# Performance work log

Measured on AMD Instinct MI355X. Metric: run time of the kernel, lower is better.

Reference implementation:

```python
import jax, jax.numpy as jnp
import numpy as np

TOTAL_DIM = 64  # 16+16+16+8+8
HIDDEN = 4 * TOTAL_DIM
NUM_HEADS = 8


def _fourier(x, num_freqs):
    # Dyadic Fourier features: sin/cos of 2^j * x for j in [0, num_freqs).
    # Output dim = input_dim * num_freqs * 2 (matches embed_dim in the module).
    freqs = 2.0 ** jnp.arange(num_freqs, dtype=x.dtype)  # (F,)
    phase = x[..., :, None] * freqs                       # (..., in, F)
    out = jnp.concatenate([jnp.sin(phase), jnp.cos(phase)], axis=-1)  # (..., in, 2F)
    return out.reshape(x.shape[:-1] + (-1,))


def setup_inputs() -> dict:
    key = jax.random.key(0)
    k1, k2, k3, k4, k5, k6 = jax.random.split(key, 6)
    B, Nq, Nk, D = 8, 256, 256, 10
    query_states = jax.random.normal(k1, (B, Nq, D), dtype=jnp.float32)
    key_states = jax.random.normal(k2, (B, Nk, D), dtype=jnp.float32)
    W1 = jax.random.normal(k3, (TOTAL_DIM, HIDDEN), dtype=jnp.float32) / np.sqrt(TOTAL_DIM)
    b1 = jnp.zeros((HIDDEN,), dtype=jnp.float32)
    W2 = jax.random.normal(k4, (HIDDEN, NUM_HEADS), dtype=jnp.float32) / np.sqrt(HIDDEN)
    b2 = jnp.zeros((NUM_HEADS,), dtype=jnp.float32)
    return {"query_states": query_states, "key_states": key_states,
            "W1": W1, "b1": b1, "W2": W2, "b2": b2}


def _features(query_states, key_states):
    # Slice per-ship fields, then broadcast pairwise: q -> (B,Nq,1,*), k -> (B,1,Nk,*)
    q_team = query_states[:, :, None, 0]          # (B,Nq,1)
    k_team = key_states[:, None, :, 0]            # (B,1,Nk)
    q_pos = query_states[:, :, None, 3:5]
    k_pos = key_states[:, None, :, 3:5]
    q_vel = query_states[:, :, None, 5:7]
    k_vel = key_states[:, None, :, 5:7]
    q_att = query_states[:, :, None, 7:9]
    k_att = key_states[:, None, :, 7:9]

    delta_pos = k_pos - q_pos                     # (B,Nq,Nk,2)
    delta_vel = k_vel - q_vel                     # (B,Nq,Nk,2)
    feat_delta_input = jnp.concatenate([delta_pos, delta_vel], axis=-1)  # (B,Nq,Nk,4)

    dist_sq = jnp.sum(delta_pos ** 2, axis=-1, keepdims=True)
    dist = jnp.sqrt(dist_sq + 1e-6)
    inv_dist = 1.0 / (dist + 0.1)
    feat_dist_input = jnp.concatenate([dist, inv_dist], axis=-1)         # (B,Nq,Nk,2)

    bearing = delta_pos / (dist + 1e-6)
    ata = jnp.sum(bearing * q_att, axis=-1, keepdims=True)
    aspect = jnp.sum(bearing * k_att, axis=-1, keepdims=True)
    feat_angle_input = jnp.concatenate([ata, aspect], axis=-1)           # (B,Nq,Nk,2)

    dot_dp_dv = jnp.sum(delta_pos * delta_vel, axis=-1, keepdims=True)
    speed_sq = jnp.sum(delta_vel ** 2, axis=-1, keepdims=True)
    ttca = jnp.tanh(jax.nn.relu(-dot_dp_dv / (speed_sq + 1e-6)))
    feat_intercept_input = jnp.concatenate([ttca, dist], axis=-1)        # (B,Nq,Nk,2)

    same_team = (q_team == k_team).astype(query_states.dtype)[..., None]
    q_speed = jnp.linalg.norm(q_vel, axis=-1, keepdims=True)
    k_speed = jnp.linalg.norm(k_vel, axis=-1, keepdims=True)
    delta_speed = k_speed - q_speed
    feat_team_input = jnp.concatenate([same_team, delta_speed], axis=-1)  # (B,Nq,Nk,2)

    out_dist = _fourier(feat_dist_input, 4)        # 16
    out_angle = _fourier(feat_angle_input, 4)      # 16
    out_delta = _fourier(feat_delta_input, 2)      # 16
    out_intercept = _fourier(feat_intercept_input, 2)  # 8
    out_team = _fourier(feat_team_input, 2)        # 8
    return jnp.concatenate([out_dist, out_angle, out_delta, out_intercept, out_team], axis=-1)


def reference(query_states, key_states, W1, b1, W2, b2):
    combined = _features(query_states, key_states)          # (B,Nq,Nk,64)
    h = jax.nn.silu(combined @ W1 + b1)                     # (B,Nq,Nk,256)
    bias = h @ W2 + b2                                      # (B,Nq,Nk,H)
    return jnp.transpose(bias, (0, 3, 1, 2))                # (B,H,Nq,Nk)
```

## Files before the change

kernel.cpp:

```cpp
#include <hip/hip_runtime.h>
#include <math.h>

#define NB 8
#define NQ 256
#define NK 256
#define DIN 10
#define FDIM 64
#define HIDDEN 256
#define NH 8
#define ROWS_PER_BLK 4

#define FSTRIDE 64
#define HSTRIDE 264

typedef float f32x4 __attribute__((ext_vector_type(4)));
typedef float f32x2 __attribute__((ext_vector_type(2)));
typedef short bf16x8 __attribute__((ext_vector_type(8)));

__device__ __forceinline__ short f2bf(float f) {
    return (short)((__float_as_uint(f) + 0x8000u) >> 16);
}
__device__ __forceinline__ unsigned cvtpk(float a, float b) {
    unsigned r;
    asm("v_cvt_pk_bf16_f32 %0, %1, %2" : "=v"(r) : "v"(a), "v"(b));
    return r;
}
__device__ __forceinline__ float rcpf(float x) { return __builtin_amdgcn_rcpf(x); }
__device__ __forceinline__ float ex2f(float x) { return __builtin_amdgcn_exp2f(x); }
__device__ __forceinline__ float sqtf(float x) { return __builtin_amdgcn_sqrtf(x); }

__device__ __forceinline__ void four4(float x, float* dst) {
    float s1 = __sinf(x), c1 = __cosf(x);
    float s2 = 2.f * s1 * c1, c2 = 1.f - 2.f * s1 * s1;
    float s4 = 2.f * s2 * c2, c4 = 1.f - 2.f * s2 * s2;
    float s8 = 2.f * s4 * c4, c8 = 1.f - 2.f * s4 * s4;
    dst[0] = s1; dst[1] = s2; dst[2] = s4; dst[3] = s8;
    dst[4] = c1; dst[5] = c2; dst[6] = c4; dst[7] = c8;
}
__device__ __forceinline__ void four2(float x, float* dst) {
    float s1 = __sinf(x), c1 = __cosf(x);
    dst[0] = s1; dst[1] = 2.f * s1 * c1;
    dst[2] = c1; dst[3] = 1.f - 2.f * s1 * s1;
}

__global__ __launch_bounds__(512, 4) void relfeat_mfma_kernel(
    const float* __restrict__ q, const float* __restrict__ k,
    const float* __restrict__ W1, const float* __restrict__ b1,
    const float* __restrict__ W2, const float* __restrict__ b2,
    float* __restrict__ out)
{
    __shared__ __align__(16) short feat_s[NK * FSTRIDE];
    __shared__ __align__(16) short h_s[64 * HSTRIDE];

    const int t = threadIdx.x;
    const int wave = t >> 6;
    const int lane15 = t & 15;
    const int quad = (t >> 4) & 3;
    const int p = t & 255;
    const int half = t >> 8;
    const int b = blockIdx.x >> 6;
    const int i0 = (blockIdx.x & 63) * ROWS_PER_BLK;

    const float* kp = k + ((size_t)b * NK + p) * DIN;
    const float k0 = kp[0], k3 = kp[3], k4 = kp[4], k5 = kp[5], k6 = kp[6],
                k7 = kp[7], k8 = kp[8];
    const float k_speed = sqtf(k5 * k5 + k6 * k6);

    bf16x8 w2f[8];
    if (wave < 4) {
#pragma unroll
        for (int ks = 0; ks < 8; ++ks) {
            const float* wp = W2 + (size_t)(ks * 32 + quad * 8) * NH + (lane15 & 7);
            bf16x8 v;
#pragma unroll
            for (int e = 0; e < 8; ++e)
                v[e] = f2bf(-0.69314718f * wp[(size_t)e * NH]);
            w2f[ks] = v;
        }
    }

    const int n0 = wave * 32;
    bf16x8 w1f[2][2];
#pragma unroll
    for (int nt = 0; nt < 2; ++nt)
#pragma unroll
        for (int ks = 0; ks < 2; ++ks) {
            const float* wp = W1 + (size_t)(ks * 32 + quad * 8) * HIDDEN
                              + (n0 + nt * 16 + lane15);
            bf16x8 v;
#pragma unroll
            for (int e = 0; e < 8; ++e)
                v[e] = f2bf(-1.44269504f * wp[(size_t)e * HIDDEN]);
            w1f[nt][ks] = v;
        }
    f32x4 b1c[2];
#pragma unroll
    for (int nt = 0; nt < 2; ++nt) {
        float4 bb = *(const float4*)&b1[n0 + nt * 16 + quad * 4];
        b1c[nt] = (f32x4){-1.44269504f * bb.x, -1.44269504f * bb.y,
                          -1.44269504f * bb.z, -1.44269504f * bb.w};
    }
    const float b2v = (lane15 < NH) ? b2[lane15] : 0.f;
    float* const outp = out + ((size_t)b * NH + (lane15 & 7)) * NQ * NK
                        + wave * 16 + quad * 4;

    const int sw = p & 7;
    const int swr = lane15 & 7;
    const f32x2 one2 = {1.f, 1.f};

#pragma unroll 1
    for (int row = 0; row < ROWS_PER_BLK; ++row) {
        const int i = i0 + row;

        {
            const float* qp = q + ((size_t)b * NQ + i) * DIN;
            const float q0 = qp[0], q3 = qp[3], q4 = qp[4], q5 = qp[5],
                        q6 = qp[6], q7 = qp[7], q8 = qp[8];

            const float dpx = k3 - q3, dpy = k4 - q4;
            const float dvx = k5 - q5, dvy = k6 - q6;
            const float dist = sqtf(dpx * dpx + dpy * dpy + 1e-6f);

            float feat[32];
            if (half == 0) {
                const float inv_dist = rcpf(dist + 0.1f);
                const float dot_dp_dv = dpx * dvx + dpy * dvy;
                const float speed_sq = dvx * dvx + dvy * dvy;
                const float z = fmaxf(0.f, -dot_dp_dv * rcpf(speed_sq + 1e-6f));
                const float ttca = 1.f - 2.f * rcpf(1.f + ex2f(2.88539008f * z));
                const float q_speed = sqtf(q5 * q5 + q6 * q6);
                const float delta_speed = k_speed - q_speed;
                four4(dist,     feat + 0);
                four4(inv_dist, feat + 8);
                four2(ttca,     feat + 16);
                feat[20] = feat[0]; feat[21] = feat[1];
                feat[22] = feat[4]; feat[23] = feat[5];
                const bool st = (q0 == k0);
                feat[24] = st ? 0.84147098f : 0.f;
                feat[25] = st ? 0.90929743f : 0.f;
                feat[26] = st ? 0.54030231f : 1.f;
                feat[27] = st ? -0.41614684f : 1.f;
                four2(delta_speed, feat + 28);
            } else {
                const float inv_d2 = rcpf(dist + 1e-6f);
                const float bear_x = dpx * inv_d2, bear_y = dpy * inv_d2;
                const float ata = bear_x * q7 + bear_y * q8;
                const float aspect = bear_x * k7 + bear_y * k8;
                four4(ata,    feat + 0);
                four4(aspect, feat + 8);
                four2(dpx,    feat + 16);
                four2(dpy,    feat + 20);
                four2(dvx,    feat + 24);
                four2(dvy,    feat + 28);
            }
#pragma unroll
            for (int j = 0; j < 4; ++j) {
                const int c8 = half ? (j + 2) : (j < 2 ? j : j + 4);
                uint4 v;
                v.x = cvtpk(feat[j * 8 + 0], feat[j * 8 + 1]);
                v.y = cvtpk(feat[j * 8 + 2], feat[j * 8 + 3]);
                v.z = cvtpk(feat[j * 8 + 4], feat[j * 8 + 5]);
                v.w = cvtpk(feat[j * 8 + 6], feat[j * 8 + 7]);
                *(uint4*)&feat_s[p * FSTRIDE + ((c8 ^ sw) * 8)] = v;
            }
        }
        __syncthreads();

#pragma unroll 1
        for (int c = 0; c < 4; ++c) {
            const int p0 = c * 64;

            f32x4 acc[2][4];
#pragma unroll
            for (int mt = 0; mt < 4; ++mt) {
                const int r2 = p0 + mt * 16 + lane15;
                const bf16x8 fb = *(const bf16x8*)
                    &feat_s[r2 * FSTRIDE + ((quad ^ swr) * 8)];
                acc[0][mt] = __builtin_amdgcn_mfma_f32_16x16x32_bf16(
                    w1f[0][0], fb, b1c[0], 0, 0, 0);
                acc[1][mt] = __builtin_amdgcn_mfma_f32_16x16x32_bf16(
                    w1f[1][0], fb, b1c[1], 0, 0, 0);
            }
#pragma unroll
            for (int mt = 0; mt < 4; ++mt) {
                const int r2 = p0 + mt * 16 + lane15;
                const bf16x8 fb = *(const bf16x8*)
                    &feat_s[r2 * FSTRIDE + (((4 + quad) ^ swr) * 8)];
#pragma unroll
                for (int nt = 0; nt < 2; ++nt)
                    acc[nt][mt] = __builtin_amdgcn_mfma_f32_16x16x32_bf16(
                        w1f[nt][1], fb, acc[nt][mt], 0, 0, 0);
            }

            uint2 pk[2][4];
#pragma unroll
            for (int nt = 0; nt < 2; ++nt)
#pragma unroll
                for (int mt = 0; mt < 4; ++mt) {
                    const f32x4 a = acc[nt][mt];
                    const f32x2 a01 = {a[0], a[1]}, a23 = {a[2], a[3]};
                    const f32x2 e01 = {ex2f(a[0]), ex2f(a[1])};
                    const f32x2 e23 = {ex2f(a[2]), ex2f(a[3])};
                    const f32x2 t01 = e01 + one2;
                    const f32x2 t23 = e23 + one2;
                    const f32x2 r01 = {rcpf(t01[0]), rcpf(t01[1])};
                    const f32x2 r23 = {rcpf(t23[0]), rcpf(t23[1])};
                    const f32x2 s01 = a01 * r01;
                    const f32x2 s23 = a23 * r23;
                    pk[nt][mt].x = cvtpk(s01[0], s01[1]);
                    pk[nt][mt].y = cvtpk(s23[0], s23[1]);
                }

            __syncthreads();

#pragma unroll
            for (int nt = 0; nt < 2; ++nt)
#pragma unroll
                for (int mt = 0; mt < 4; ++mt) {
                    const int pair = mt * 16 + lane15;
                    const int hbase = n0 + nt * 16 + quad * 4;
                    *(uint2*)&h_s[pair * HSTRIDE + hbase] = pk[nt][mt];
                }
            __syncthreads();

            if (wave < 4) {
                const int pw = wave * 16;
                f32x4 acc2 = (f32x4){b2v, b2v, b2v, b2v};
#pragma unroll
                for (int ks = 0; ks < 8; ++ks) {
                    const bf16x8 ha = *(const bf16x8*)&h_s[(pw + lane15) * HSTRIDE
                                                            + ks * 32 + quad * 8];
                    acc2 = __builtin_amdgcn_mfma_f32_16x16x32_bf16(ha, w2f[ks], acc2, 0, 0, 0);
                }
                if (lane15 < NH) {
                    float* op = outp + (size_t)i * NK + p0;
                    *(float4*)op = make_float4(acc2[0], acc2[1], acc2[2], acc2[3]);
                }
            }
        }
    }
}

extern "C" void kernel_launch(void* const* d_in, const int* in_sizes, int n_in,
                              void* d_out, int out_size, void* d_ws, size_t ws_size,
                              hipStream_t stream) {
    const float* q  = (const float*)d_in[0];
    const float* k  = (const float*)d_in[1];
    const float* W1 = (const float*)d_in[2];
    const float* b1 = (const float*)d_in[3];
    const float* W2 = (const float*)d_in[4];
    const float* b2 = (const float*)d_in[5];
    float* out = (float*)d_out;

    dim3 grid(NB * NQ / ROWS_PER_BLK);
    dim3 block(512);
    relfeat_mfma_kernel<<<grid, block, 0, stream>>>(q, k, W1, b1, W2, b2, out);
}
```

Measured before the change: 107.7 us.

## Double-buffer hidden activations and defer second GEMM to overlap with next chunk

The hidden-activation LDS buffer is split into two, and each chunk's second GEMM (W2 projection plus output store) is deferred into the next chunk's iteration, where it runs alongside the first GEMM. This removes one block-wide barrier per chunk and lets the W2 MFMAs overlap the W1 MFMAs and SiLU work of the following chunk. Rows per block go from 4 to 8, which halves the grid, and the launch bounds now target 2 waves per EU. The extra LDS for the second buffer and the smaller grid reduce how many blocks fit per CU, which can cost latency hiding.

```diff
diff --git a/kernel.cpp b/kernel.cpp
--- a/kernel.cpp
+++ b/kernel.cpp
@@ -8,7 +8,7 @@
 #define FDIM 64
 #define HIDDEN 256
 #define NH 8
-#define ROWS_PER_BLK 4
+#define ROWS_PER_BLK 8
 
 #define FSTRIDE 64
 #define HSTRIDE 264
@@ -43,14 +43,16 @@
     dst[2] = c1; dst[3] = 1.f - 2.f * s1 * s1;
 }
 
-__global__ __launch_bounds__(512, 4) void relfeat_mfma_kernel(
+__global__ __attribute__((amdgpu_flat_work_group_size(512, 512),
+                          amdgpu_waves_per_eu(2, 2)))
+void relfeat_mfma_kernel(
     const float* __restrict__ q, const float* __restrict__ k,
     const float* __restrict__ W1, const float* __restrict__ b1,
     const float* __restrict__ W2, const float* __restrict__ b2,
     float* __restrict__ out)
 {
     __shared__ __align__(16) short feat_s[NK * FSTRIDE];
-    __shared__ __align__(16) short h_s[64 * HSTRIDE];
+    __shared__ __align__(16) short hbuf[2][64 * HSTRIDE];
 
     const int t = threadIdx.x;
     const int wave = t >> 6;
@@ -58,8 +60,8 @@
     const int quad = (t >> 4) & 3;
     const int p = t & 255;
     const int half = t >> 8;
-    const int b = blockIdx.x >> 6;
-    const int i0 = (blockIdx.x & 63) * ROWS_PER_BLK;
+    const int b = blockIdx.x >> 5;
+    const int i0 = (blockIdx.x & 31) * ROWS_PER_BLK;
 
     const float* kp = k + ((size_t)b * NK + p) * DIN;
     const float k0 = kp[0], k3 = kp[3], k4 = kp[4], k5 = kp[5], k6 = kp[6],
@@ -107,6 +109,24 @@
     const int sw = p & 7;
     const int swr = lane15 & 7;
     const f32x2 one2 = {1.f, 1.f};
+
+    auto gemm2 = [&](int oi, int op0, int pb) {
+        const short* hb = hbuf[pb];
+        const int pw = wave * 16;
+        f32x4 acc2 = (f32x4){b2v, b2v, b2v, b2v};
+#pragma unroll
+        for (int ks = 0; ks < 8; ++ks) {
+            const bf16x8 ha = *(const bf16x8*)&hb[(pw + lane15) * HSTRIDE
+                                                  + ks * 32 + quad * 8];
+            acc2 = __builtin_amdgcn_mfma_f32_16x16x32_bf16(ha, w2f[ks], acc2, 0, 0, 0);
+        }
+        if (lane15 < NH) {
+            float* op = outp + (size_t)oi * NK + op0;
+            *(float4*)op = make_float4(acc2[0], acc2[1], acc2[2], acc2[3]);
+        }
+    };
+
+    int pend_i = -1, pend_p0 = 0, pend_b = 0;
 
 #pragma unroll 1
     for (int row = 0; row < ROWS_PER_BLK; ++row) {
@@ -169,6 +189,10 @@
 #pragma unroll 1
         for (int c = 0; c < 4; ++c) {
             const int p0 = c * 64;
+            const int wb = c & 1;
+
+            if (wave < 4 && pend_i >= 0)
+                gemm2(pend_i, pend_p0, pend_b);
 
             f32x4 acc[2][4];
 #pragma unroll
@@ -192,7 +216,6 @@
                         w1f[nt][1], fb, acc[nt][mt], 0, 0, 0);
             }
 
-            uint2 pk[2][4];
 #pragma unroll
             for (int nt = 0; nt < 2; ++nt)
 #pragma unroll
@@ -207,38 +230,21 @@
                     const f32x2 r23 = {rcpf(t23[0]), rcpf(t23[1])};
                     const f32x2 s01 = a01 * r01;
                     const f32x2 s23 = a23 * r23;
-                    pk[nt][mt].x = cvtpk(s01[0], s01[1]);
-                    pk[nt][mt].y = cvtpk(s23[0], s23[1]);
-                }
-
-            __syncthreads();
-
-#pragma unroll
-            for (int nt = 0; nt < 2; ++nt)
-#pragma unroll
-                for (int mt = 0; mt < 4; ++mt) {
+                    uint2 pk;
+                    pk.x = cvtpk(s01[0], s01[1]);
+                    pk.y = cvtpk(s23[0], s23[1]);
                     const int pair = mt * 16 + lane15;
                     const int hbase = n0 + nt * 16 + quad * 4;
-                    *(uint2*)&h_s[pair * HSTRIDE + hbase] = pk[nt][mt];
+                    *(uint2*)&hbuf[wb][pair * HSTRIDE + hbase] = pk;
                 }
+
             __syncthreads();
 
-            if (wave < 4) {
-                const int pw = wave * 16;
-                f32x4 acc2 = (f32x4){b2v, b2v, b2v, b2v};
-#pragma unroll
-                for (int ks = 0; ks < 8; ++ks) {
-                    const bf16x8 ha = *(const bf16x8*)&h_s[(pw + lane15) * HSTRIDE
-                                                            + ks * 32 + quad * 8];
-                    acc2 = __builtin_amdgcn_mfma_f32_16x16x32_bf16(ha, w2f[ks], acc2, 0, 0, 0);
-                }
-                if (lane15 < NH) {
-                    float* op = outp + (size_t)i * NK + p0;
-                    *(float4*)op = make_float4(acc2[0], acc2[1], acc2[2], acc2[3]);
-                }
-            }
+            pend_i = i; pend_p0 = p0; pend_b = wb;
         }
     }
+    if (wave < 4)
+        gemm2(pend_i, pend_p0, pend_b);
 }
 
 extern "C" void kernel_launch(void* const* d_in, const int* in_sizes, int n_in,
```

Result: slower. 112.2 us (+4.1%).
